# Kernel optimization log

Measured on AMD Instinct MI355X. Metric: run time of the kernel, lower is better.

The kernel has to match this reference:

```python
import jax, jax.numpy as jnp
import numpy as np

DIM = 1024      # transformer hidden size
HEADS = 16
HD = DIM // HEADS
FF = 2048       # ff_dim = 2*dim (default)
E = 128         # char_embedding_dim
V = 256         # char vocab
SHRINK = 5
NLAYERS = 6
HALF = DIM // 2
NEG = -1e9


def _ln(x, g, b):
    m = x.mean(-1, keepdims=True)
    v = ((x - m) ** 2).mean(-1, keepdims=True)
    return (x - m) / jnp.sqrt(v + 1e-12) * g + b


def setup_inputs() -> dict:
    key = jax.random.key(0)
    ks = iter(jax.random.split(key, 64))
    B, S, SRC = 32, 1000, 256
    d = {}
    d["encoder_states"] = jax.random.normal(next(ks), (B, SRC, DIM), jnp.float32)
    d["encoder_mask"] = jnp.ones((B, SRC), jnp.float32)
    d["target_ids"] = jax.random.randint(next(ks), (B, S), 0, V)
    d["target_mask"] = jnp.ones((B, S), jnp.float32)

    def p(shape):
        return jax.random.normal(next(ks), shape, jnp.float32) * 0.02

    d["char_emb"] = p((V, E))
    d["pre_pos_emb"] = p((1, 1024, E))
    d["Wc"] = p((E, DIM)); d["bc"] = jnp.zeros((DIM,))
    d["bert_pos_emb"] = p((512, DIM)); d["bert_tok_emb"] = p((DIM,))
    d["emb_ln_g"] = jnp.ones((DIM,)); d["emb_ln_b"] = jnp.zeros((DIM,))
    L = NLAYERS
    d["Wqkv"] = p((L, DIM, 3 * DIM)); d["bqkv"] = jnp.zeros((L, 3 * DIM))
    d["Wo"] = p((L, DIM, DIM)); d["bo"] = jnp.zeros((L, DIM))
    d["ln1_g"] = jnp.ones((L, DIM)); d["ln1_b"] = jnp.zeros((L, DIM))
    d["Cq"] = p((L, DIM, DIM)); d["cbq"] = jnp.zeros((L, DIM))
    d["Ckv"] = p((L, DIM, 2 * DIM)); d["cbkv"] = jnp.zeros((L, 2 * DIM))
    d["Co"] = p((L, DIM, DIM)); d["cbo"] = jnp.zeros((L, DIM))
    d["ln2_g"] = jnp.ones((L, DIM)); d["ln2_b"] = jnp.zeros((L, DIM))
    d["W1"] = p((L, DIM, FF)); d["b1"] = jnp.zeros((L, FF))
    d["W2"] = p((L, FF, DIM)); d["b2"] = jnp.zeros((L, DIM))
    d["ln3_g"] = jnp.ones((L, DIM)); d["ln3_b"] = jnp.zeros((L, DIM))
    d["Wnar"] = p((DIM, SHRINK * HALF)); d["bnar"] = jnp.zeros((SHRINK * HALF,))
    d["W_ih"] = p((4 * DIM, E + HALF)); d["W_hh"] = p((4 * DIM, DIM))
    d["b_ih"] = jnp.zeros((4 * DIM,)); d["b_hh"] = jnp.zeros((4 * DIM,))
    d["Wout"] = p((HALF + DIM, V)); d["bout"] = jnp.zeros((V,))
    return d


def reference(encoder_states, encoder_mask, target_ids, target_mask,
              char_emb, pre_pos_emb, Wc, bc, bert_pos_emb, bert_tok_emb,
              emb_ln_g, emb_ln_b, Wqkv, bqkv, Wo, bo, ln1_g, ln1_b,
              Cq, cbq, Ckv, cbkv, Co, cbo, ln2_g, ln2_b,
              W1, b1, W2, b2, ln3_g, ln3_b, Wnar, bnar,
              W_ih, W_hh, b_ih, b_hh, Wout, bout):
    B, S = target_ids.shape
    # _hidden_states (training): prepend SHRINK ones, drop last SHRINK chars
    dec_input = jnp.concatenate([jnp.ones((B, SHRINK), target_ids.dtype), target_ids[:, :-SHRINK]], 1)
    input_mask = jnp.concatenate([jnp.ones((B, SHRINK), target_mask.dtype), target_mask[:, :-SHRINK]], 1)
    emb = char_emb[dec_input] + pre_pos_emb[0, :S]            # [B,S,E]
    # CharToPseudoWord (position-wise proj + max-pool over shrink window)
    h = jax.nn.relu(emb @ Wc + bc) * input_mask[..., None]
    T = S // SHRINK
    pooled = h.reshape(B, T, SHRINK, DIM).max(2)               # [B,T,D]
    smask = input_mask.reshape(B, T, SHRINK).max(2)            # [B,T]
    # Bert embeddings layer (inputs_embeds + pos + token-type, LN)
    x = _ln(pooled + bert_pos_emb[:T] + bert_tok_emb, emb_ln_g, emb_ln_b)
    causal = jnp.tril(jnp.ones((T, T), bool))
    self_bias = jnp.where(causal, 0.0, NEG)[None, None] + (1.0 - smask)[:, None, None, :] * NEG
    cross_bias = (1.0 - encoder_mask)[:, None, None, :] * NEG
    scale = 1.0 / np.sqrt(HD)

    def heads(t):
        return t.reshape(B, -1, HEADS, HD).transpose(0, 2, 1, 3)

    def merge(t):
        return t.transpose(0, 2, 1, 3).reshape(B, -1, DIM)

    for l in range(NLAYERS):
        q, k, v = jnp.split(x @ Wqkv[l] + bqkv[l], 3, axis=-1)
        a = jax.nn.softmax(jnp.einsum('bhqd,bhkd->bhqk', heads(q), heads(k)) * scale + self_bias, -1)
        o = merge(jnp.einsum('bhqk,bhkd->bhqd', a, heads(v))) @ Wo[l] + bo[l]
        x = _ln(x + o, ln1_g[l], ln1_b[l])
        q = x @ Cq[l] + cbq[l]
        k, v = jnp.split(encoder_states @ Ckv[l] + cbkv[l], 2, axis=-1)
        a = jax.nn.softmax(jnp.einsum('bhqd,bhkd->bhqk', heads(q), heads(k)) * scale + cross_bias, -1)
        o = merge(jnp.einsum('bhqk,bhkd->bhqd', a, heads(v))) @ Co[l] + cbo[l]
        x = _ln(x + o, ln2_g[l], ln2_b[l])
        f = jax.nn.relu(x @ W1[l] + b1[l]) @ W2[l] + b2[l]
        x = _ln(x + f, ln3_g[l], ln3_b[l])

    # nar_proj -> per-char states [B,S,D/2]
    char_states = (x @ Wnar + bnar).reshape(B, T * SHRINK, HALF)[:, :S]
    # char LSTM over full target sequence (carried state == chunked python loop)
    pad_in = jnp.concatenate([jnp.ones((B, 1), target_ids.dtype), target_ids], 1)[:, :S]
    lstm_in = jnp.concatenate([char_emb[pad_in], char_states], -1)   # [B,S,E+D/2]

    def step(carry, xt):
        h, c = carry
        g = xt @ W_ih.T + h @ W_hh.T + b_ih + b_hh
        i, f, gg, o = jnp.split(g, 4, axis=-1)
        c = jax.nn.sigmoid(f) * c + jax.nn.sigmoid(i) * jnp.tanh(gg)
        h = jax.nn.sigmoid(o) * jnp.tanh(c)
        return (h, c), h

    h0 = jnp.zeros((B, DIM), lstm_in.dtype)
    _, hs = jax.lax.scan(step, (h0, h0), lstm_in.transpose(1, 0, 2))
    lstm_out = hs.transpose(1, 0, 2)                                  # [B,S,D]
    logits = jnp.concatenate([lstm_out, char_states], -1) @ Wout + bout
    logp = jax.nn.log_softmax(logits, -1)
    nll = -jnp.take_along_axis(logp, target_ids[..., None], 2)[..., 0]
    return (nll * target_mask).sum() / target_mask.sum()
```

## Files before the change

### kernel.cpp

```cpp
#include <hip/hip_runtime.h>
#include <cstdint>
#include <cstddef>

#define DEV __device__ __forceinline__

typedef unsigned short u16;
typedef __attribute__((ext_vector_type(8))) short short8;
typedef __attribute__((ext_vector_type(4))) float floatx4;

DEV float bf2f(u16 h) { union { unsigned u; float f; } c; c.u = ((unsigned)h) << 16; return c.f; }
DEV u16 f2bf(float f) {
  union { float f; unsigned u; } c; c.f = f;
  unsigned r = 0x7fffu + ((c.u >> 16) & 1u);
  return (u16)((c.u + r) >> 16);
}
DEV short8 ld8(const u16* p) { return *(const short8*)p; }
DEV floatx4 mfma16(short8 a, short8 b, floatx4 c) {
  return __builtin_amdgcn_mfma_f32_16x16x32_bf16(a, b, c, 0, 0, 0);
}
DEV void async16(const u16* g, u16* l) {
  __builtin_amdgcn_global_load_lds((__attribute__((address_space(1))) void*)(uintptr_t)(const void*)g,
                                   (__attribute__((address_space(3))) void*)(uintptr_t)(void*)l, 16, 0, 0);
}
DEV float sigm(float x) { return 1.f / (1.f + __expf(-x)); }

DEV float blk_sum256(float v) {
  __shared__ float sh[4];
  #pragma unroll
  for (int d = 32; d >= 1; d >>= 1) v += __shfl_xor(v, d, 64);
  if ((threadIdx.x & 63) == 0) sh[threadIdx.x >> 6] = v;
  __syncthreads();
  v = sh[0] + sh[1] + sh[2] + sh[3];
  __syncthreads();
  return v;
}

template<bool RELU, bool WF32, bool WBF16, bool ACC>
__global__ __launch_bounds__(256, 2) void gemm_kernel(
    const u16* __restrict__ A, const u16* __restrict__ BT,
    const float* __restrict__ bias, float* __restrict__ Cf, u16* __restrict__ Cb,
    int M, int N, int K, int lda, int ldb, int ldc)
{
  __shared__ u16 As[4096];
  __shared__ u16 Bs[4096];
  const int tid = threadIdx.x;
  const int lane = tid & 63;
  const int w = tid >> 6;
  const int nTiles = N >> 7;
  const int bm = blockIdx.x / nTiles;
  const int bn = blockIdx.x - bm * nTiles;
  const int m0 = bm << 7, n0 = bn << 7;
  const int q = lane >> 4, lm = lane & 15;
  const int wm = (w & 1) << 6, wn = (w >> 1) << 6;

  const int s1 = tid, s2 = tid + 256;
  const int r1 = s1 >> 2, c1 = (s1 & 3) ^ ((r1 >> 2) & 3);
  const int r2 = s2 >> 2, c2 = (s2 & 3) ^ ((r2 >> 2) & 3);
  const u16* ga1 = A + (size_t)(m0 + r1) * lda + c1 * 8;
  const u16* ga2 = A + (size_t)(m0 + r2) * lda + c2 * 8;
  const u16* gb1 = BT + (size_t)(n0 + r1) * ldb + c1 * 8;
  const u16* gb2 = BT + (size_t)(n0 + r2) * ldb + c2 * 8;

  floatx4 acc[4][4] = {};

  for (int kt = 0; kt < K; kt += 32) {
    async16(ga1 + kt, &As[s1 * 8]);
    async16(ga2 + kt, &As[s2 * 8]);
    async16(gb1 + kt, &Bs[s1 * 8]);
    async16(gb2 + kt, &Bs[s2 * 8]);
    __syncthreads();
    short8 af[4], bfr[4];
    #pragma unroll
    for (int i = 0; i < 4; ++i) {
      int r = wm + i * 16 + lm;
      af[i] = ld8(&As[(r * 4 + (q ^ ((r >> 2) & 3))) * 8]);
      r = wn + i * 16 + lm;
      bfr[i] = ld8(&Bs[(r * 4 + (q ^ ((r >> 2) & 3))) * 8]);
    }
    #pragma unroll
    for (int mi = 0; mi < 4; ++mi)
      #pragma unroll
      for (int ni = 0; ni < 4; ++ni)
        acc[mi][ni] = mfma16(af[mi], bfr[ni], acc[mi][ni]);
    __syncthreads();
  }
  #pragma unroll
  for (int ni = 0; ni < 4; ++ni) {
    int col = n0 + wn + ni * 16 + lm;
    float bv = ACC ? 0.f : bias[col];
    #pragma unroll
    for (int mi = 0; mi < 4; ++mi) {
      int rowb = m0 + wm + mi * 16 + q * 4;
      #pragma unroll
      for (int r = 0; r < 4; ++r) {
        float v = acc[mi][ni][r] + bv;
        if (RELU) v = fmaxf(v, 0.f);
        size_t idx = (size_t)(rowb + r) * ldc + col;
        if (WF32) { if (ACC) Cf[idx] += v; else Cf[idx] = v; }
        if (WBF16) Cb[idx] = f2bf(v);
      }
    }
  }
}

__global__ __launch_bounds__(256) void cvt_transpose_kernel(
    const float* __restrict__ src, u16* __restrict__ dst, int K, int N)
{
  __shared__ float tile[32][33];
  int n0 = blockIdx.x * 32, k0 = blockIdx.y * 32;
  int tx = threadIdx.x & 31, ty = threadIdx.x >> 5;
  #pragma unroll
  for (int i = 0; i < 32; i += 8)
    tile[ty + i][tx] = src[(size_t)(k0 + ty + i) * N + n0 + tx];
  __syncthreads();
  #pragma unroll
  for (int i = 0; i < 32; i += 8)
    dst[(size_t)(n0 + ty + i) * K + k0 + tx] = f2bf(tile[tx][ty + i]);
}

__global__ void cvt_kernel(const float* __restrict__ s, u16* __restrict__ d, int n) {
  int i = blockIdx.x * 256 + threadIdx.x;
  int stride = gridDim.x * 256;
  for (; i < n; i += stride) d[i] = f2bf(s[i]);
}

__global__ void cvt_perm_kernel(const float* __restrict__ src, u16* __restrict__ dst, int cols) {
  int qrow = blockIdx.x;
  int orig = (qrow & 3) * 1024 + (qrow >> 2);
  const float* sp = src + (size_t)orig * cols;
  u16* dp = dst + (size_t)qrow * cols;
  for (int c = threadIdx.x; c < cols; c += 256) dp[c] = f2bf(sp[c]);
}

__global__ void bias_perm_kernel(const float* __restrict__ bih, const float* __restrict__ bhh,
                                 float* __restrict__ bsum) {
  int q = blockIdx.x * 256 + threadIdx.x;
  int orig = (q & 3) * 1024 + (q >> 2);
  bsum[q] = bih[orig] + bhh[orig];
}

__global__ void embed_kernel(const int* __restrict__ tgt, const float* __restrict__ ce,
                             const float* __restrict__ pp, u16* __restrict__ out) {
  int row = blockIdx.x;
  int b = row / 1000, s = row - b * 1000;
  int id = (s < 5) ? 1 : tgt[b * 1000 + s - 5];
  int e = threadIdx.x;
  out[(size_t)row * 128 + e] = f2bf(ce[id * 128 + e] + pp[s * 128 + e]);
}

__global__ __launch_bounds__(256) void pool_bert_ln_kernel(
    const u16* __restrict__ hb, const float* __restrict__ tmask,
    const float* __restrict__ pos, const float* __restrict__ tok,
    const float* __restrict__ g, const float* __restrict__ bt,
    float* __restrict__ x, u16* __restrict__ xb, float* __restrict__ smaskOut)
{
  int row = blockIdx.x, b = row / 200, t = row - b * 200;
  int tid = threadIdx.x;
  float m[4] = {0.f, 0.f, 0.f, 0.f};
  float sm = 0.f;
  for (int wi = 0; wi < 5; ++wi) {
    int s = t * 5 + wi;
    float im = (s < 5) ? 1.f : tmask[b * 1000 + s - 5];
    sm = fmaxf(sm, im);
    const u16* hr = hb + (size_t)(b * 1000 + s) * 1024;
    #pragma unroll
    for (int i = 0; i < 4; ++i) {
      int d = tid + i * 256;
      m[i] = fmaxf(m[i], bf2f(hr[d]) * im);
    }
  }
  float y[4]; float ssum = 0.f;
  #pragma unroll
  for (int i = 0; i < 4; ++i) {
    int d = tid + i * 256;
    y[i] = m[i] + pos[t * 1024 + d] + tok[d];
    ssum += y[i];
  }
  float mean = blk_sum256(ssum) * (1.f / 1024.f);
  float vs = 0.f;
  #pragma unroll
  for (int i = 0; i < 4; ++i) { float dd = y[i] - mean; vs += dd * dd; }
  float var = blk_sum256(vs) * (1.f / 1024.f);
  float rs = rsqrtf(var + 1e-12f);
  #pragma unroll
  for (int i = 0; i < 4; ++i) {
    int d = tid + i * 256;
    float o = (y[i] - mean) * rs * g[d] + bt[d];
    x[(size_t)row * 1024 + d] = o;
    xb[(size_t)row * 1024 + d] = f2bf(o);
  }
  if (tid == 0) smaskOut[row] = sm;
}

__global__ __launch_bounds__(256) void resid_ln_kernel(
    float* __restrict__ x, const float* __restrict__ o,
    const float* __restrict__ g, const float* __restrict__ bt,
    u16* __restrict__ xb)
{
  size_t row = blockIdx.x;
  int tid = threadIdx.x;
  float y[4]; float s = 0.f;
  #pragma unroll
  for (int i = 0; i < 4; ++i) {
    int d = tid + i * 256;
    y[i] = x[row * 1024 + d] + o[row * 1024 + d];
    s += y[i];
  }
  float mean = blk_sum256(s) * (1.f / 1024.f);
  float vs = 0.f;
  #pragma unroll
  for (int i = 0; i < 4; ++i) { float dd = y[i] - mean; vs += dd * dd; }
  float var = blk_sum256(vs) * (1.f / 1024.f);
  float rs = rsqrtf(var + 1e-12f);
  #pragma unroll
  for (int i = 0; i < 4; ++i) {
    int d = tid + i * 256;
    float out = (y[i] - mean) * rs * g[d] + bt[d];
    x[row * 1024 + d] = out;
    xb[row * 1024 + d] = f2bf(out);
  }
}

__global__ __launch_bounds__(256) void scores_kernel(
    const u16* __restrict__ Q, int qstride,
    const u16* __restrict__ Kp, int kstride, int kcoff, int krows,
    const float* __restrict__ mask, u16* __restrict__ P, int selfmode)
{
  int wid = blockIdx.x * 4 + (threadIdx.x >> 6);
  int lane = threadIdx.x & 63;
  int qt = wid % 13, h = (wid / 13) & 15, b = wid / 208;
  int lm = lane & 15, quad = lane >> 4;
  int t0 = qt * 16;
  int trow = t0 + lm; if (trow > 199) trow = 199;
  const u16* qp = Q + (size_t)(b * 200 + trow) * qstride + h * 64;
  short8 a0 = ld8(qp + quad * 8);
  short8 a1 = ld8(qp + 32 + quad * 8);
  floatx4 S[16];
  const int nmf = selfmode ? 13 : 16;
  for (int ut = 0; ut < nmf; ++ut) {
    int ur = ut * 16 + lm; if (ur >= krows) ur = krows - 1;
    const u16* kp = Kp + (size_t)(b * krows + ur) * kstride + kcoff + h * 64;
    floatx4 z = {0.f, 0.f, 0.f, 0.f};
    z = mfma16(a0, ld8(kp + quad * 8), z);
    z = mfma16(a1, ld8(kp + 32 + quad * 8), z);
    S[ut] = z;
  }
  for (int ut = nmf; ut < 16; ++ut) S[ut] = (floatx4){0.f, 0.f, 0.f, 0.f};
  const float scale = 0.125f;
  u16* prow_base = P + (size_t)((b * 16 + h) * 200) * 256;
  for (int r = 0; r < 4; ++r) {
    int t = t0 + quad * 4 + r;
    float mx = -3e38f;
    float vv[16];
    #pragma unroll
    for (int ut = 0; ut < 16; ++ut) {
      int u = ut * 16 + lm;
      float bias;
      if (selfmode) {
        bias = ((u <= t && u < 200) ? 0.f : -1e9f);
        if (u < 200) bias += (1.f - mask[b * 200 + u]) * -1e9f;
      } else {
        bias = (1.f - mask[b * 256 + u]) * -1e9f;
      }
      float v = S[ut][r] * scale + bias;
      vv[ut] = v;
      mx = fmaxf(mx, v);
    }
    #pragma unroll
    for (int d = 1; d < 16; d <<= 1) mx = fmaxf(mx, __shfl_xor(mx, d, 64));
    float sum = 0.f;
    #pragma unroll
    for (int ut = 0; ut < 16; ++ut) { float e = __expf(vv[ut] - mx); vv[ut] = e; sum += e; }
    #pragma unroll
    for (int d = 1; d < 16; d <<= 1) sum += __shfl_xor(sum, d, 64);
    float inv = 1.f / sum;
    if (t < 200) {
      u16* pr = prow_base + (size_t)t * 256;
      #pragma unroll
      for (int ut = 0; ut < 16; ++ut) pr[ut * 16 + lm] = f2bf(vv[ut] * inv);
    }
  }
}

__global__ __launch_bounds__(256) void vtrans_kernel(
    const u16* __restrict__ src, int stride, int coff, int krows, u16* __restrict__ vT)
{
  int b = blockIdx.x >> 4, h = blockIdx.x & 15;
  __shared__ u16 tile[64][257];
  for (int idx = threadIdx.x; idx < 256 * 64; idx += 256) {
    int u = idx >> 6, d = idx & 63;
    u16 v = 0;
    if (u < krows) v = src[(size_t)(b * krows + u) * stride + coff + h * 64 + d];
    tile[d][u] = v;
  }
  __syncthreads();
  u16* dst = vT + (size_t)((b * 16 + h) * 64) * 256;
  for (int idx = threadIdx.x; idx < 64 * 256; idx += 256) {
    int d = idx >> 8, u = idx & 255;
    dst[(size_t)d * 256 + u] = tile[d][u];
  }
}

__global__ __launch_bounds__(256) void pv_kernel(
    const u16* __restrict__ P, const u16* __restrict__ vT, u16* __restrict__ O)
{
  int wid = blockIdx.x * 4 + (threadIdx.x >> 6);
  int lane = threadIdx.x & 63;
  int qt = wid % 13, h = (wid / 13) & 15, b = wid / 208;
  int lm = lane & 15, quad = lane >> 4;
  int t0 = qt * 16;
  int trow = t0 + lm; if (trow > 199) trow = 199;
  const u16* prow = P + ((size_t)((b * 16 + h) * 200) + trow) * 256;
  const u16* vbase = vT + (size_t)((b * 16 + h) * 64) * 256;
  floatx4 acc[4] = {};
  #pragma unroll
  for (int kb = 0; kb < 8; ++kb) {
    short8 a = ld8(prow + kb * 32 + quad * 8);
    #pragma unroll
    for (int dn = 0; dn < 4; ++dn) {
      short8 bb = ld8(vbase + (size_t)(dn * 16 + lm) * 256 + kb * 32 + quad * 8);
      acc[dn] = mfma16(a, bb, acc[dn]);
    }
  }
  #pragma unroll
  for (int dn = 0; dn < 4; ++dn)
    #pragma unroll
    for (int r = 0; r < 4; ++r) {
      int t = t0 + quad * 4 + r;
      if (t < 200)
        O[(size_t)(b * 200 + t) * 1024 + h * 64 + dn * 16 + lm] = f2bf(acc[dn][r]);
    }
}

__global__ void lstmin_kernel(const int* __restrict__ tgt, const float* __restrict__ ce,
                              const u16* __restrict__ cs, u16* __restrict__ out) {
  int row = blockIdx.x;
  int b = row / 1000, s = row - b * 1000;
  int c = threadIdx.x;
  u16 v;
  if (c < 128) {
    int id = (s == 0) ? 1 : tgt[b * 1000 + s - 1];
    v = f2bf(ce[id * 128 + c]);
  } else {
    v = cs[(size_t)row * 512 + (c - 128)];
  }
  out[(size_t)(s * 32 + b) * 640 + c] = v;
}

__global__ __launch_bounds__(256, 1) void lstm_kernel(
    const u16* __restrict__ xproj, const u16* __restrict__ Wp,
    u16* __restrict__ hbuf, float* __restrict__ cbuf, u16* __restrict__ lout,
    unsigned* __restrict__ flags, int t0, int nsteps)
{
  __shared__ u16 smem[32768];
  float* g_all = (float*)smem;

  const int tid = threadIdx.x;
  const int lane = tid & 63;
  const int w = tid >> 6;
  const int bk = blockIdx.x;
  const int lm = lane & 15, quad = lane >> 4;
  const int Q0 = bk * 64;

  short8 wfrag[32];
  #pragma unroll
  for (int kk = 0; kk < 32; ++kk)
    wfrag[kk] = ld8(Wp + (size_t)(Q0 + w * 16 + lm) * 1024 + kk * 32 + quad * 8);

  const int b_ = tid >> 3;
  const int u0 = (tid & 7) * 2;
  float c0 = 0.f, c1 = 0.f;
  if (t0 == 0) {
    *(unsigned*)&hbuf[b_ * 2048 + bk * 32 + u0] = 0u;
  } else {
    c0 = cbuf[b_ * 1024 + bk * 16 + u0];
    c1 = cbuf[b_ * 1024 + bk * 16 + u0 + 1];
  }
  __syncthreads();
  if (w == 0) {
    __builtin_amdgcn_fence(__ATOMIC_RELEASE, "agent");
    if (lane == 0)
      __hip_atomic_store(&flags[bk * 16], 1u, __ATOMIC_RELAXED, __HIP_MEMORY_SCOPE_AGENT);
  }

  for (int ltt = 0; ltt < nsteps; ++ltt) {
    const int t = t0 + ltt;

    short8 xp = ld8(xproj + (size_t)(ltt * 32 + b_) * 4096 + Q0 + u0 * 4);

    if (w == 0) {
      unsigned want = (unsigned)(ltt + 1);
      int spin = 0;
      for (;;) {
        unsigned v = __hip_atomic_load(&flags[lane * 16], __ATOMIC_RELAXED, __HIP_MEMORY_SCOPE_AGENT);
        if (__all((int)(v >= want))) break;
        if (((++spin) & 63) == 0) __builtin_amdgcn_fence(__ATOMIC_ACQUIRE, "agent");
        __builtin_amdgcn_s_sleep(1);
      }
      __builtin_amdgcn_fence(__ATOMIC_ACQUIRE, "agent");
    }
    __syncthreads();

    const u16* hsrc = hbuf + (size_t)(t & 1) * 65536;
    #pragma unroll
    for (int it = 0; it < 16; ++it) {
      int i = it * 2048 + tid * 8;
      int b = i >> 10, c = i & 1023;
      short8 v = ld8(hsrc + b * 2048 + ((c >> 4) << 5) + (c & 15));
      *(short8*)&smem[b * 1024 + (c ^ ((b & 7) * 8))] = v;
    }
    __syncthreads();

    floatx4 acc0 = {0.f, 0.f, 0.f, 0.f}, acc1 = {0.f, 0.f, 0.f, 0.f};
    #pragma unroll
    for (int kk = 0; kk < 32; ++kk) {
      int cix = kk * 32 + quad * 8;
      short8 a0 = ld8(&smem[lm * 1024 + (cix ^ ((lm & 7) * 8))]);
      short8 a1 = ld8(&smem[(16 + lm) * 1024 + (cix ^ ((lm & 7) * 8))]);
      acc0 = mfma16(a0, wfrag[kk], acc0);
      acc1 = mfma16(a1, wfrag[kk], acc1);
    }
    __syncthreads();
    #pragma unroll
    for (int r = 0; r < 4; ++r) {
      g_all[(quad * 4 + r) * 66 + w * 16 + lm] = acc0[r];
      g_all[(16 + quad * 4 + r) * 66 + w * 16 + lm] = acc1[r];
    }
    __syncthreads();

    const u16* xpp = (const u16*)&xp;
    const float* gb = g_all + b_ * 66 + u0 * 4;
    float gi = gb[0] + bf2f(xpp[0]);
    float gf = gb[1] + bf2f(xpp[1]);
    float gg = gb[2] + bf2f(xpp[2]);
    float go = gb[3] + bf2f(xpp[3]);
    c0 = sigm(gf) * c0 + sigm(gi) * tanhf(gg);
    float h0v = sigm(go) * tanhf(c0);
    gi = gb[4] + bf2f(xpp[4]);
    gf = gb[5] + bf2f(xpp[5]);
    gg = gb[6] + bf2f(xpp[6]);
    go = gb[7] + bf2f(xpp[7]);
    c1 = sigm(gf) * c1 + sigm(gi) * tanhf(gg);
    float h1v = sigm(go) * tanhf(c1);

    u16* hdst = hbuf + (size_t)((t + 1) & 1) * 65536 + b_ * 2048 + bk * 32 + u0;
    hdst[0] = f2bf(h0v);
    hdst[1] = f2bf(h1v);
    u16* lo = lout + (size_t)(b_ * 1000 + t) * 1024 + bk * 16 + u0;
    lo[0] = f2bf(h0v);
    lo[1] = f2bf(h1v);

    __syncthreads();
    if (w == 0) {
      __builtin_amdgcn_fence(__ATOMIC_RELEASE, "agent");
      if (lane == 0)
        __hip_atomic_store(&flags[bk * 16], (unsigned)(ltt + 2), __ATOMIC_RELAXED, __HIP_MEMORY_SCOPE_AGENT);
    }
  }
  cbuf[b_ * 1024 + bk * 16 + u0] = c0;
  cbuf[b_ * 1024 + bk * 16 + u0 + 1] = c1;
}

__global__ __launch_bounds__(256) void nll_kernel(
    const float* __restrict__ logits, const int* __restrict__ tgt,
    const float* __restrict__ tmask, float* __restrict__ acc)
{
  int wid = blockIdx.x * 4 + (threadIdx.x >> 6);
  int lane = threadIdx.x & 63;
  float ls = 0.f, ms = 0.f;
  for (int rr = 0; rr < 4; ++rr) {
    int row = wid * 4 + rr;
    const float* lp = logits + (size_t)row * 256;
    float v[4]; float mx = -3e38f;
    #pragma unroll
    for (int i = 0; i < 4; ++i) { v[i] = lp[lane + i * 64]; mx = fmaxf(mx, v[i]); }
    #pragma unroll
    for (int d = 1; d < 64; d <<= 1) mx = fmaxf(mx, __shfl_xor(mx, d, 64));
    float s = 0.f;
    #pragma unroll
    for (int i = 0; i < 4; ++i) s += __expf(v[i] - mx);
    #pragma unroll
    for (int d = 1; d < 64; d <<= 1) s += __shfl_xor(s, d, 64);
    float lse = mx + __logf(s);
    int tg = tgt[row];
    float tv = 0.f;
    #pragma unroll
    for (int i = 0; i < 4; ++i) if (lane + i * 64 == tg) tv = v[i];
    #pragma unroll
    for (int d = 1; d < 64; d <<= 1) tv += __shfl_xor(tv, d, 64);
    float mk = tmask[row];
    ls += (lse - tv) * mk;
    ms += mk;
  }
  if (lane == 0) { atomicAdd(&acc[0], ls); atomicAdd(&acc[1], ms); }
}

__global__ void zero_kernel(float* acc) {
  if (threadIdx.x == 0) { acc[0] = 0.f; acc[1] = 0.f; }
}
__global__ void flags_reset_kernel(unsigned* flags) {
  int i = threadIdx.x;
  #pragma unroll
  for (int k = 0; k < 4; ++k) flags[i + k * 256] = 0u;
}
__global__ void finalize_kernel(const float* acc, float* out) {
  if (threadIdx.x == 0) out[0] = acc[0] / acc[1];
}
__global__ void diag_kernel(float* out, float v) {
  if (threadIdx.x == 0) out[0] = v;
}

constexpr size_t AL(size_t x) { return (x + 255) & ~(size_t)255; }
constexpr size_t o_Wihp  = 0;
constexpr size_t o_Whhp  = AL(o_Wihp + 4096ull * 640 * 2);
constexpr size_t o_WoutT = AL(o_Whhp + 4096ull * 1024 * 2);
constexpr size_t o_bsum  = AL(o_WoutT + 256ull * 1536 * 2);
constexpr size_t o_hbuf  = AL(o_bsum + 4096ull * 4);
constexpr size_t o_cbuf  = AL(o_hbuf + 2ull * 32 * 2048 * 2);
constexpr size_t o_acc   = AL(o_cbuf + 32ull * 1024 * 4);
constexpr size_t o_flags = AL(o_acc + 256);
constexpr size_t o_smask = AL(o_flags + 4096);
constexpr size_t o_cs    = AL(o_smask + 6400ull * 4);
constexpr size_t o_lout  = AL(o_cs + 6400ull * 2560 * 2);
constexpr size_t o_arena = AL(o_lout + 32000ull * 1024 * 2);
constexpr size_t a_wl    = o_arena;
constexpr size_t wl_qkv  = a_wl;
constexpr size_t wl_wo   = wl_qkv + 3072ull * 1024 * 2;
constexpr size_t wl_cq   = wl_wo + 1024ull * 1024 * 2;
constexpr size_t wl_ckv  = wl_cq + 1024ull * 1024 * 2;
constexpr size_t wl_co   = wl_ckv + 2048ull * 1024 * 2;
constexpr size_t wl_w1   = wl_co + 1024ull * 1024 * 2;
constexpr size_t wl_w2   = wl_w1 + 2048ull * 1024 * 2;
constexpr size_t a_enc   = AL(wl_w2 + 2048ull * 1024 * 2);
constexpr size_t a_x     = AL(a_enc + 8192ull * 1024 * 2);
constexpr size_t a_xbf   = AL(a_x + 6400ull * 1024 * 4);
constexpr size_t a_scr   = AL(a_xbf + 6400ull * 1024 * 2);
constexpr size_t s_qkv   = a_scr;
constexpr size_t s_kvc   = s_qkv + 6400ull * 1024 * 2;
constexpr size_t s_P     = AL(a_scr + 46661632ull);
constexpr size_t s_vT    = AL(s_P + 32ull * 16 * 200 * 256 * 2);
constexpr size_t s_S2    = AL(s_vT + 32ull * 16 * 64 * 256 * 2);
constexpr size_t s_o32   = AL(s_S2 + 6400ull * 2048 * 2);
constexpr size_t a_endA  = AL(s_o32 + 6400ull * 1024 * 4);
constexpr size_t s_emb   = a_scr;
constexpr size_t s_hbf   = a_scr + 32000ull * 128 * 2;
constexpr size_t b_lin   = o_arena;
constexpr size_t b_xpj   = b_lin + 32000ull * 640 * 2;
constexpr size_t b_end   = AL(b_xpj + 16000ull * 4096 * 2);
constexpr size_t WS_NEED = (a_endA > b_end ? a_endA : b_end);

extern "C" void kernel_launch(void* const* d_in, const int* in_sizes, int n_in,
                              void* d_out, int out_size, void* d_ws, size_t ws_size,
                              hipStream_t stream)
{
  if (ws_size < WS_NEED) {
    diag_kernel<<<dim3(1), dim3(64), 0, stream>>>((float*)d_out, (float)(ws_size >> 20));
    return;
  }
  const float* enc     = (const float*)d_in[0];
  const float* encmask = (const float*)d_in[1];
  const int*   tgt     = (const int*)d_in[2];
  const float* tmask   = (const float*)d_in[3];
  const float* char_emb= (const float*)d_in[4];
  const float* pre_pos = (const float*)d_in[5];
  const float* Wc      = (const float*)d_in[6];
  const float* bc      = (const float*)d_in[7];
  const float* bert_pos= (const float*)d_in[8];
  const float* bert_tok= (const float*)d_in[9];
  const float* eln_g   = (const float*)d_in[10];
  const float* eln_b   = (const float*)d_in[11];
  const float* Wqkv    = (const float*)d_in[12];
  const float* bqkv    = (const float*)d_in[13];
  const float* Wo      = (const float*)d_in[14];
  const float* bo      = (const float*)d_in[15];
  const float* ln1g    = (const float*)d_in[16];
  const float* ln1b    = (const float*)d_in[17];
  const float* Cq      = (const float*)d_in[18];
  const float* cbq     = (const float*)d_in[19];
  const float* Ckv     = (const float*)d_in[20];
  const float* cbkv    = (const float*)d_in[21];
  const float* Co      = (const float*)d_in[22];
  const float* cbo     = (const float*)d_in[23];
  const float* ln2g    = (const float*)d_in[24];
  const float* ln2b    = (const float*)d_in[25];
  const float* W1      = (const float*)d_in[26];
  const float* b1      = (const float*)d_in[27];
  const float* W2      = (const float*)d_in[28];
  const float* b2      = (const float*)d_in[29];
  const float* ln3g    = (const float*)d_in[30];
  const float* ln3b    = (const float*)d_in[31];
  const float* Wnar    = (const float*)d_in[32];
  const float* bnar    = (const float*)d_in[33];
  const float* W_ih    = (const float*)d_in[34];
  const float* W_hh    = (const float*)d_in[35];
  const float* b_ih    = (const float*)d_in[36];
  const float* b_hh    = (const float*)d_in[37];
  const float* Wout    = (const float*)d_in[38];
  const float* bout    = (const float*)d_in[39];

  char* ws = (char*)d_ws;
  auto U = [&](size_t off) -> u16* { return (u16*)(ws + off); };
  auto F = [&](size_t off) -> float* { return (float*)(ws + off); };

  float* accum = F(o_acc);
  unsigned* flags = (unsigned*)(ws + o_flags);
  zero_kernel<<<dim3(1), dim3(64), 0, stream>>>(accum);

  auto gemm = [&](const u16* A, const u16* BT, const float* bias, float* Cf, u16* Cb,
                  int M, int N, int K, int lda, int ldb, int ldc, int relu, int accf) {
    dim3 grid((M / 128) * (N / 128));
    if (Cb && relu)
      gemm_kernel<true, false, true, false><<<grid, 256, 0, stream>>>(A, BT, bias, nullptr, Cb, M, N, K, lda, ldb, ldc);
    else if (Cb)
      gemm_kernel<false, false, true, false><<<grid, 256, 0, stream>>>(A, BT, bias, nullptr, Cb, M, N, K, lda, ldb, ldc);
    else if (accf)
      gemm_kernel<false, true, false, true><<<grid, 256, 0, stream>>>(A, BT, bias, Cf, nullptr, M, N, K, lda, ldb, ldc);
    else
      gemm_kernel<false, true, false, false><<<grid, 256, 0, stream>>>(A, BT, bias, Cf, nullptr, M, N, K, lda, ldb, ldc);
  };

  cvt_perm_kernel<<<dim3(4096), 256, 0, stream>>>(W_ih, U(o_Wihp), 640);
  cvt_perm_kernel<<<dim3(4096), 256, 0, stream>>>(W_hh, U(o_Whhp), 1024);
  bias_perm_kernel<<<dim3(16), 256, 0, stream>>>(b_ih, b_hh, F(o_bsum));
  cvt_transpose_kernel<<<dim3(8, 48), 256, 0, stream>>>(Wout, U(o_WoutT), 1536, 256);
  cvt_kernel<<<dim3(4096), 256, 0, stream>>>(enc, U(a_enc), 32 * 256 * 1024);

  cvt_transpose_kernel<<<dim3(32, 4), 256, 0, stream>>>(Wc, U(a_wl), 128, 1024);
  embed_kernel<<<dim3(32000), dim3(128), 0, stream>>>(tgt, char_emb, pre_pos, U(s_emb));
  gemm(U(s_emb), U(a_wl), bc, nullptr, U(s_hbf), 32000, 1024, 128, 128, 128, 1024, 1, 0);
  pool_bert_ln_kernel<<<dim3(6400), 256, 0, stream>>>(
      U(s_hbf), tmask, bert_pos, bert_tok, eln_g, eln_b, F(a_x), U(a_xbf), F(o_smask));

  for (int l = 0; l < 6; ++l) {
    cvt_transpose_kernel<<<dim3(96, 32), 256, 0, stream>>>(Wqkv + (size_t)l * 1024 * 3072, U(wl_qkv), 1024, 3072);
    cvt_transpose_kernel<<<dim3(32, 32), 256, 0, stream>>>(Wo + (size_t)l * 1024 * 1024, U(wl_wo), 1024, 1024);
    cvt_transpose_kernel<<<dim3(32, 32), 256, 0, stream>>>(Cq + (size_t)l * 1024 * 1024, U(wl_cq), 1024, 1024);
    cvt_transpose_kernel<<<dim3(64, 32), 256, 0, stream>>>(Ckv + (size_t)l * 1024 * 2048, U(wl_ckv), 1024, 2048);
    cvt_transpose_kernel<<<dim3(32, 32), 256, 0, stream>>>(Co + (size_t)l * 1024 * 1024, U(wl_co), 1024, 1024);
    cvt_transpose_kernel<<<dim3(64, 32), 256, 0, stream>>>(W1 + (size_t)l * 1024 * 2048, U(wl_w1), 1024, 2048);
    cvt_transpose_kernel<<<dim3(32, 64), 256, 0, stream>>>(W2 + (size_t)l * 2048 * 1024, U(wl_w2), 2048, 1024);

    gemm(U(a_xbf), U(wl_qkv), bqkv + l * 3072, nullptr, U(s_qkv), 6400, 3072, 1024, 1024, 1024, 3072, 0, 0);
    vtrans_kernel<<<dim3(512), 256, 0, stream>>>(U(s_qkv), 3072, 2048, 200, U(s_vT));
    scores_kernel<<<dim3(1664), 256, 0, stream>>>(
        U(s_qkv), 3072, U(s_qkv), 3072, 1024, 200, F(o_smask), U(s_P), 1);
    pv_kernel<<<dim3(1664), 256, 0, stream>>>(U(s_P), U(s_vT), U(s_S2));
    gemm(U(s_S2), U(wl_wo), bo + l * 1024, F(s_o32), nullptr, 6400, 1024, 1024, 1024, 1024, 1024, 0, 0);
    resid_ln_kernel<<<dim3(6400), 256, 0, stream>>>(F(a_x), F(s_o32), ln1g + l * 1024, ln1b + l * 1024, U(a_xbf));

    gemm(U(a_xbf), U(wl_cq), cbq + l * 1024, nullptr, U(s_qkv), 6400, 1024, 1024, 1024, 1024, 1024, 0, 0);
    gemm(U(a_enc), U(wl_ckv), cbkv + l * 2048, nullptr, U(s_kvc), 8192, 2048, 1024, 1024, 1024, 2048, 0, 0);
    vtrans_kernel<<<dim3(512), 256, 0, stream>>>(U(s_kvc), 2048, 1024, 256, U(s_vT));
    scores_kernel<<<dim3(1664), 256, 0, stream>>>(
        U(s_qkv), 1024, U(s_kvc), 2048, 0, 256, encmask, U(s_P), 0);
    pv_kernel<<<dim3(1664), 256, 0, stream>>>(U(s_P), U(s_vT), U(s_S2));
    gemm(U(s_S2), U(wl_co), cbo + l * 1024, F(s_o32), nullptr, 6400, 1024, 1024, 1024, 1024, 1024, 0, 0);
    resid_ln_kernel<<<dim3(6400), 256, 0, stream>>>(F(a_x), F(s_o32), ln2g + l * 1024, ln2b + l * 1024, U(a_xbf));

    gemm(U(a_xbf), U(wl_w1), b1 + l * 2048, nullptr, U(s_S2), 6400, 2048, 1024, 1024, 1024, 2048, 1, 0);
    gemm(U(s_S2), U(wl_w2), b2 + l * 1024, F(s_o32), nullptr, 6400, 1024, 2048, 2048, 2048, 1024, 0, 0);
    resid_ln_kernel<<<dim3(6400), 256, 0, stream>>>(F(a_x), F(s_o32), ln3g + l * 1024, ln3b + l * 1024, U(a_xbf));
  }

  cvt_transpose_kernel<<<dim3(80, 32), 256, 0, stream>>>(Wnar, U(a_wl), 1024, 2560);
  gemm(U(a_xbf), U(a_wl), bnar, nullptr, U(o_cs), 6400, 2560, 1024, 1024, 1024, 2560, 0, 0);

  lstmin_kernel<<<dim3(32000), dim3(640), 0, stream>>>(tgt, char_emb, U(o_cs), U(b_lin));

  for (int c = 0; c < 2; ++c) {
    gemm(U(b_lin) + (size_t)c * 16000 * 640, U(o_Wihp), F(o_bsum), nullptr, U(b_xpj),
         16000, 4096, 640, 640, 640, 4096, 0, 0);
    flags_reset_kernel<<<dim3(1), 256, 0, stream>>>(flags);
    const u16* xprojp = U(b_xpj);
    const u16* Wpp = U(o_Whhp);
    u16* hbufp = U(o_hbuf);
    float* cbufp = F(o_cbuf);
    u16* loutp = U(o_lout);
    unsigned* flagsp = flags;
    int t0 = c * 500, ns = 500;
    void* kargs[] = { &xprojp, &Wpp, &hbufp, &cbufp, &loutp, &flagsp, &t0, &ns };
    hipLaunchCooperativeKernel(lstm_kernel, dim3(64), dim3(256), kargs, 0u, stream);
  }

  gemm(U(o_lout), U(o_WoutT), bout, F(b_xpj), nullptr, 32000, 256, 1024, 1024, 1536, 256, 0, 0);
  gemm(U(o_cs), U(o_WoutT) + 1024, nullptr, F(b_xpj), nullptr, 32000, 256, 512, 512, 1536, 256, 0, 1);
  nll_kernel<<<dim3(2000), 256, 0, stream>>>(F(b_xpj), tgt, tmask, accum);
  finalize_kernel<<<dim3(1), dim3(64), 0, stream>>>(accum, (float*)d_out);
}
```

Before: 14.68 ms.

## Store LSTM hidden states time-major and read previous step directly from output

```diff
diff --git a/kernel.cpp b/kernel.cpp
--- a/kernel.cpp
+++ b/kernel.cpp
@@ -333,7 +333,8 @@
 }
 
 __global__ void lstmin_kernel(const int* __restrict__ tgt, const float* __restrict__ ce,
-                              const u16* __restrict__ cs, u16* __restrict__ out) {
+                              const u16* __restrict__ cs, u16* __restrict__ out,
+                              u16* __restrict__ cst) {
   int row = blockIdx.x;
   int b = row / 1000, s = row - b * 1000;
   int c = threadIdx.x;
@@ -343,14 +344,15 @@
     v = f2bf(ce[id * 128 + c]);
   } else {
     v = cs[(size_t)row * 512 + (c - 128)];
+    cst[(size_t)(s * 32 + b) * 512 + (c - 128)] = v;
   }
   out[(size_t)(s * 32 + b) * 640 + c] = v;
 }
 
 __global__ __launch_bounds__(256, 1) void lstm_kernel(
     const u16* __restrict__ xproj, const u16* __restrict__ Wp,
-    u16* __restrict__ hbuf, float* __restrict__ cbuf, u16* __restrict__ lout,
-    unsigned* __restrict__ flags, int t0, int nsteps)
+    u16* __restrict__ lout, const u16* __restrict__ zbuf,
+    float* __restrict__ cbuf, unsigned* __restrict__ flags, int t0, int nsteps)
 {
   __shared__ u16 smem[32768];
   float* g_all = (float*)smem;
@@ -370,43 +372,36 @@
   const int b_ = tid >> 3;
   const int u0 = (tid & 7) * 2;
   float c0 = 0.f, c1 = 0.f;
-  if (t0 == 0) {
-    *(unsigned*)&hbuf[b_ * 2048 + bk * 32 + u0] = 0u;
-  } else {
+  if (t0 != 0) {
     c0 = cbuf[b_ * 1024 + bk * 16 + u0];
     c1 = cbuf[b_ * 1024 + bk * 16 + u0 + 1];
   }
-  __syncthreads();
-  if (w == 0) {
-    __builtin_amdgcn_fence(__ATOMIC_RELEASE, "agent");
-    if (lane == 0)
-      __hip_atomic_store(&flags[bk * 16], 1u, __ATOMIC_RELAXED, __HIP_MEMORY_SCOPE_AGENT);
-  }
 
   for (int ltt = 0; ltt < nsteps; ++ltt) {
     const int t = t0 + ltt;
 
     short8 xp = ld8(xproj + (size_t)(ltt * 32 + b_) * 4096 + Q0 + u0 * 4);
 
-    if (w == 0) {
-      unsigned want = (unsigned)(ltt + 1);
-      int spin = 0;
-      for (;;) {
-        unsigned v = __hip_atomic_load(&flags[lane * 16], __ATOMIC_RELAXED, __HIP_MEMORY_SCOPE_AGENT);
-        if (__all((int)(v >= want))) break;
-        if (((++spin) & 63) == 0) __builtin_amdgcn_fence(__ATOMIC_ACQUIRE, "agent");
-        __builtin_amdgcn_s_sleep(1);
+    if (ltt > 0) {
+      if (w == 0) {
+        unsigned want = (unsigned)ltt;
+        int spin = 0;
+        for (;;) {
+          unsigned v = __hip_atomic_load(&flags[lane * 16], __ATOMIC_RELAXED, __HIP_MEMORY_SCOPE_AGENT);
+          if (__all((int)(v >= want))) break;
+          if (((++spin) & 1023) == 0) __builtin_amdgcn_fence(__ATOMIC_ACQUIRE, "agent");
+          __builtin_amdgcn_s_sleep(1);
+        }
       }
-      __builtin_amdgcn_fence(__ATOMIC_ACQUIRE, "agent");
-    }
-    __syncthreads();
-
-    const u16* hsrc = hbuf + (size_t)(t & 1) * 65536;
+      __syncthreads();
+    }
+
+    const u16* hsrc = (t == 0) ? zbuf : (lout + (size_t)(t - 1) * 32768);
     #pragma unroll
     for (int it = 0; it < 16; ++it) {
       int i = it * 2048 + tid * 8;
       int b = i >> 10, c = i & 1023;
-      short8 v = ld8(hsrc + b * 2048 + ((c >> 4) << 5) + (c & 15));
+      short8 v = ld8(hsrc + (size_t)b * 1024 + c);
       *(short8*)&smem[b * 1024 + (c ^ ((b & 7) * 8))] = v;
     }
     __syncthreads();
@@ -443,18 +438,15 @@
     c1 = sigm(gf) * c1 + sigm(gi) * tanhf(gg);
     float h1v = sigm(go) * tanhf(c1);
 
-    u16* hdst = hbuf + (size_t)((t + 1) & 1) * 65536 + b_ * 2048 + bk * 32 + u0;
-    hdst[0] = f2bf(h0v);
-    hdst[1] = f2bf(h1v);
-    u16* lo = lout + (size_t)(b_ * 1000 + t) * 1024 + bk * 16 + u0;
-    lo[0] = f2bf(h0v);
-    lo[1] = f2bf(h1v);
+    unsigned hval = ((unsigned)f2bf(h1v) << 16) | (unsigned)f2bf(h0v);
+    unsigned* hdst = (unsigned*)(lout + (size_t)t * 32768 + b_ * 1024 + bk * 16 + u0);
+    __hip_atomic_store(hdst, hval, __ATOMIC_RELAXED, __HIP_MEMORY_SCOPE_AGENT);
 
     __syncthreads();
     if (w == 0) {
       __builtin_amdgcn_fence(__ATOMIC_RELEASE, "agent");
       if (lane == 0)
-        __hip_atomic_store(&flags[bk * 16], (unsigned)(ltt + 2), __ATOMIC_RELAXED, __HIP_MEMORY_SCOPE_AGENT);
+        __hip_atomic_store(&flags[bk * 16], (unsigned)(ltt + 1), __ATOMIC_RELAXED, __HIP_MEMORY_SCOPE_AGENT);
     }
   }
   cbuf[b_ * 1024 + bk * 16 + u0] = c0;
@@ -470,6 +462,7 @@
   float ls = 0.f, ms = 0.f;
   for (int rr = 0; rr < 4; ++rr) {
     int row = wid * 4 + rr;
+    int bix = (row & 31) * 1000 + (row >> 5);
     const float* lp = logits + (size_t)row * 256;
     float v[4]; float mx = -3e38f;
     #pragma unroll
@@ -482,13 +475,13 @@
     #pragma unroll
     for (int d = 1; d < 64; d <<= 1) s += __shfl_xor(s, d, 64);
     float lse = mx + __logf(s);
-    int tg = tgt[row];
+    int tg = tgt[bix];
     float tv = 0.f;
     #pragma unroll
     for (int i = 0; i < 4; ++i) if (lane + i * 64 == tg) tv = v[i];
     #pragma unroll
     for (int d = 1; d < 64; d <<= 1) tv += __shfl_xor(tv, d, 64);
-    float mk = tmask[row];
+    float mk = tmask[bix];
     ls += (lse - tv) * mk;
     ms += mk;
   }
@@ -502,6 +495,9 @@
   int i = threadIdx.x;
   #pragma unroll
   for (int k = 0; k < 4; ++k) flags[i + k * 256] = 0u;
+}
+__global__ void zfill_kernel(unsigned* p) {
+  p[blockIdx.x * 256 + threadIdx.x] = 0u;
 }
 __global__ void finalize_kernel(const float* acc, float* out) {
   if (threadIdx.x == 0) out[0] = acc[0] / acc[1];
@@ -515,8 +511,8 @@
 constexpr size_t o_Whhp  = AL(o_Wihp + 4096ull * 640 * 2);
 constexpr size_t o_WoutT = AL(o_Whhp + 4096ull * 1024 * 2);
 constexpr size_t o_bsum  = AL(o_WoutT + 256ull * 1536 * 2);
-constexpr size_t o_hbuf  = AL(o_bsum + 4096ull * 4);
-constexpr size_t o_cbuf  = AL(o_hbuf + 2ull * 32 * 2048 * 2);
+constexpr size_t o_zbuf  = AL(o_bsum + 4096ull * 4);
+constexpr size_t o_cbuf  = AL(o_zbuf + 65536);
 constexpr size_t o_acc   = AL(o_cbuf + 32ull * 1024 * 4);
 constexpr size_t o_flags = AL(o_acc + 256);
 constexpr size_t o_smask = AL(o_flags + 4096);
@@ -546,7 +542,8 @@
 constexpr size_t s_hbf   = a_scr + 32000ull * 128 * 2;
 constexpr size_t b_lin   = o_arena;
 constexpr size_t b_xpj   = b_lin + 32000ull * 640 * 2;
-constexpr size_t b_end   = AL(b_xpj + 16000ull * 4096 * 2);
+constexpr size_t o_cst   = AL(b_xpj + 16000ull * 4096 * 2);
+constexpr size_t b_end   = AL(o_cst + 32000ull * 512 * 2);
 constexpr size_t WS_NEED = (a_endA > b_end ? a_endA : b_end);
 
 extern "C" void kernel_launch(void* const* d_in, const int* in_sizes, int n_in,
@@ -605,6 +602,7 @@
   float* accum = F(o_acc);
   unsigned* flags = (unsigned*)(ws + o_flags);
   zero_kernel<<<dim3(1), dim3(64), 0, stream>>>(accum);
+  zfill_kernel<<<dim3(64), 256, 0, stream>>>((unsigned*)(ws + o_zbuf));
 
   auto gemm = [&](const u16* A, const u16* BT, const float* bias, float* Cf, u16* Cb,
                   int M, int N, int K, int lda, int ldb, int ldc, int relu, int accf) {
@@ -665,7 +663,7 @@
   cvt_transpose_kernel<<<dim3(80, 32), 256, 0, stream>>>(Wnar, U(a_wl), 1024, 2560);
   gemm(U(a_xbf), U(a_wl), bnar, nullptr, U(o_cs), 6400, 2560, 1024, 1024, 1024, 2560, 0, 0);
 
-  lstmin_kernel<<<dim3(32000), dim3(640), 0, stream>>>(tgt, char_emb, U(o_cs), U(b_lin));
+  lstmin_kernel<<<dim3(32000), dim3(640), 0, stream>>>(tgt, char_emb, U(o_cs), U(b_lin), U(o_cst));
 
   for (int c = 0; c < 2; ++c) {
     gemm(U(b_lin) + (size_t)c * 16000 * 640, U(o_Wihp), F(o_bsum), nullptr, U(b_xpj),
@@ -673,17 +671,17 @@
     flags_reset_kernel<<<dim3(1), 256, 0, stream>>>(flags);
     const u16* xprojp = U(b_xpj);
     const u16* Wpp = U(o_Whhp);
-    u16* hbufp = U(o_hbuf);
+    u16* loutp = U(o_lout);
+    const u16* zbufp = U(o_zbuf);
     float* cbufp = F(o_cbuf);
-    u16* loutp = U(o_lout);
     unsigned* flagsp = flags;
     int t0 = c * 500, ns = 500;
-    void* kargs[] = { &xprojp, &Wpp, &hbufp, &cbufp, &loutp, &flagsp, &t0, &ns };
+    void* kargs[] = { &xprojp, &Wpp, &loutp, &zbufp, &cbufp, &flagsp, &t0, &ns };
     hipLaunchCooperativeKernel(lstm_kernel, dim3(64), dim3(256), kargs, 0u, stream);
   }
 
   gemm(U(o_lout), U(o_WoutT), bout, F(b_xpj), nullptr, 32000, 256, 1024, 1024, 1536, 256, 0, 0);
-  gemm(U(o_cs), U(o_WoutT) + 1024, nullptr, F(b_xpj), nullptr, 32000, 256, 512, 512, 1536, 256, 0, 1);
+  gemm(U(o_cst), U(o_WoutT) + 1024, nullptr, F(b_xpj), nullptr, 32000, 256, 512, 512, 1536, 256, 0, 1);
   nll_kernel<<<dim3(2000), 256, 0, stream>>>(F(b_xpj), tgt, tmask, accum);
   finalize_kernel<<<dim3(1), dim3(64), 0, stream>>>(accum, (float*)d_out);
 }
```

Result: faster. 13.31 ms (-9.3%).
